# Performance work log

Measured on AMD Instinct MI355X. Metric: run time of the kernel, lower is better.

The kernel has to match this reference:

```python
import jax, jax.numpy as jnp
import numpy as np

B, C, N, H = 4, 512, 16384, 8
D = C // H
EPS = 1e-6

def setup_inputs() -> dict:
    key = jax.random.key(0)
    k1, k2, k3 = jax.random.split(key, 3)
    # xavier_normal std for Linear(C, out): sqrt(2/(fan_in+fan_out))
    std_qkv = (2.0 / (C + 3 * C)) ** 0.5
    std_proj = (2.0 / (C + C)) ** 0.5
    return {
        "x": jax.random.normal(k1, (B, C, N), dtype=jnp.float32),
        "W_qkv": jax.random.normal(k2, (C, 3 * C), dtype=jnp.float32) * std_qkv,
        "b_qkv": jnp.zeros((3 * C,), dtype=jnp.float32),
        "W_proj": jax.random.normal(k3, (C, C), dtype=jnp.float32) * std_proj,
        "b_proj": jnp.zeros((C,), dtype=jnp.float32),
    }

def _phi(x):
    return jax.nn.elu(x) + 1.0

def reference(x, W_qkv, b_qkv, W_proj, b_proj):
    # x: [B, C, N] -> [B, N, C]
    xt = jnp.swapaxes(x, 1, 2)
    qkv = xt @ W_qkv + b_qkv                      # [B, N, 3C]
    q, k, v = jnp.split(qkv, 3, axis=-1)
    # [B, N, C] -> [B, H, N, D]
    def heads(t):
        return jnp.swapaxes(t.reshape(B, N, H, D), 1, 2)
    q, k, v = heads(q), heads(k), heads(v)
    q_phi = _phi(q)                               # [B, H, N, D]
    k_phi = _phi(k)
    S = jnp.einsum('bhnd,bhne->bhde', k_phi, v)   # [B, H, D, D] KV state
    k_sum = k_phi.sum(axis=-2)                    # [B, H, D]
    num = jnp.einsum('bhnd,bhde->bhne', q_phi, S) # [B, H, N, D]
    den = jnp.einsum('bhnd,bhd->bhn', q_phi, k_sum)[..., None] + EPS
    out = num / den                               # [B, H, N, D]
    out = jnp.swapaxes(out, 1, 2).reshape(B, N, C)
    out = out @ W_proj + b_proj                   # [B, N, C]
    return jnp.swapaxes(out, 1, 2)                # [B, C, N]
```

## Files before the change

kernel.cpp:

```cpp
#include <hip/hip_runtime.h>
#include <cmath>

#define B_  4
#define C_  512
#define N_  16384
#define H_  8
#define D_  64
#define C3_ 1536
#define EPS 1e-6f

#define PADA 72
#define PADT 136
#define PADO 132

typedef __attribute__((ext_vector_type(8))) short bf16x8;
typedef __attribute__((ext_vector_type(4))) float f32x4;

typedef const void __attribute__((address_space(1)))* gas_t;
typedef void __attribute__((address_space(3)))* las_t;

__device__ __forceinline__ void gld16(const void* g, void* l) {
    __builtin_amdgcn_global_load_lds((gas_t)(unsigned long long)g,
                                     (las_t)(unsigned)(unsigned long long)l,
                                     16, 0, 0);
}

__device__ __forceinline__ ushort f2bf(float f) {
    union { float f; unsigned u; } c{f};
    unsigned r = (c.u + 0x7FFF + ((c.u >> 16) & 1)) >> 16;
    return (ushort)r;
}
__device__ __forceinline__ float bf2f(ushort b) {
    union { unsigned u; float f; } c{(unsigned)b << 16};
    return c.f;
}
__device__ __forceinline__ float phi_f(float x) { return x > 0.f ? x + 1.f : __expf(x); }

__global__ __launch_bounds__(256) void k_transpose(
        const float* __restrict__ src, ushort* __restrict__ dst,
        int R, int Cc, long sStride, long dStride) {
    __shared__ ushort T[64][72];
    const long sb = (long)blockIdx.z * sStride;
    const long db = (long)blockIdx.z * dStride;
    const int c0 = blockIdx.x * 64, r0 = blockIdx.y * 64;
    const int t = threadIdx.x;
    const int ct = t & 15, rt = t >> 4;
    float4 v[4];
    #pragma unroll
    for (int k = 0; k < 4; ++k)
        v[k] = *(const float4*)(src + sb + (long)(r0 + rt * 4 + k) * Cc + c0 + ct * 4);
    #pragma unroll
    for (int j = 0; j < 4; ++j) {
        ushort pk[4];
        #pragma unroll
        for (int k = 0; k < 4; ++k) pk[k] = f2bf(((const float*)&v[k])[j]);
        *(uint2*)&T[ct * 4 + j][rt * 4] = *(uint2*)pk;
    }
    __syncthreads();
    const int c = t >> 2, rq = (t & 3) * 16;
    ushort* d = dst + db + (long)(c0 + c) * R + r0 + rq;
    *(int4*)(d)     = *(const int4*)&T[c][rq];
    *(int4*)(d + 8) = *(const int4*)&T[c][rq + 8];
}

__global__ __launch_bounds__(256) void k_kv_s(
        const ushort* __restrict__ xt, const ushort* __restrict__ Wqt,
        const float* __restrict__ bqkv, float* __restrict__ S_g,
        float* __restrict__ ksum_g) {
    const int s = blockIdx.x, h = blockIdx.y, b = blockIdx.z;
    const int tid = threadIdx.x;
    const int w = tid >> 6, ln = tid & 63, lr = ln & 15, lq = ln >> 4;
    const int bh = b * H_ + h;
    const int lrow = ln >> 3;
    const int csw  = (ln & 7) ^ lrow;
    const int sw   = lr & 7;

    __shared__ __align__(16) char smem[34816];
    ushort* AxL = (ushort*)smem;
    ushort* BwL = (ushort*)(smem + 16384);
    ushort (*kvT)[PADT] = (ushort(*)[PADT])smem;
    __shared__ float biasL[128];

    if (tid < 128) {
        int col = tid < 64 ? (512 + h * 64 + tid) : (1024 + h * 64 + (tid - 64));
        biasL[tid] = bqkv[col];
    }

    int gA[4], gB[4];
    #pragma unroll
    for (int i = 0; i < 4; ++i) {
        const int row = (w * 4 + i) * 8 + lrow;
        gA[i] = row * C_ + csw * 8;
        const int wr = row < 64 ? (512 + h * 64 + row) : (1024 + h * 64 + (row - 64));
        gB[i] = wr * C_ + csw * 8;
    }
    const long xb = (long)b * N_ * C_;

    const f32x4 FZ = {0.f, 0.f, 0.f, 0.f};
    f32x4 Sacc[4] = {FZ, FZ, FZ, FZ};
    f32x4 Kacc = FZ;
    bf16x8 ONES;
    #pragma unroll
    for (int i = 0; i < 8; ++i) ONES[i] = (short)0x3F80;

    for (int it = 0; it < 4; ++it) {
        const ushort* xa = xt + xb + (long)((s * 4 + it) * 128) * C_;
        f32x4 acc[2][8];
        #pragma unroll
        for (int mi = 0; mi < 2; mi++)
            #pragma unroll
            for (int ji = 0; ji < 8; ji++) acc[mi][ji] = FZ;

        for (int kc = 0; kc < 8; ++kc) {
            const int c0 = kc * 64;
            __syncthreads();
            #pragma unroll
            for (int i = 0; i < 4; ++i) {
                const int ch = w * 4 + i;
                gld16(xa + gA[i] + c0, AxL + ch * 512);
                gld16(Wqt + gB[i] + c0, BwL + ch * 512);
            }
            __syncthreads();
            #pragma unroll
            for (int ks = 0; ks < 2; ++ks) {
                const int cof = ((ks * 4 + lq) ^ sw) * 8;
                bf16x8 a[2], bb[8];
                #pragma unroll
                for (int mi = 0; mi < 2; mi++)
                    a[mi] = *(const bf16x8*)&AxL[(w * 32 + mi * 16 + lr) * 64 + cof];
                #pragma unroll
                for (int ji = 0; ji < 8; ji++)
                    bb[ji] = *(const bf16x8*)&BwL[(ji * 16 + lr) * 64 + cof];
                #pragma unroll
                for (int mi = 0; mi < 2; mi++)
                    #pragma unroll
                    for (int ji = 0; ji < 8; ji++)
                        acc[mi][ji] = __builtin_amdgcn_mfma_f32_16x16x32_bf16(
                            a[mi], bb[ji], acc[mi][ji], 0, 0, 0);
            }
        }
        __syncthreads();
        #pragma unroll
        for (int mi = 0; mi < 2; mi++) {
            int nl = w * 32 + mi * 16 + lq * 4;
            #pragma unroll
            for (int ji = 0; ji < 8; ji++) {
                int j = ji * 16 + lr;
                float bs = biasL[j];
                ushort pk[4];
                #pragma unroll
                for (int r = 0; r < 4; r++) {
                    float vv = acc[mi][ji][r] + bs;
                    if (j < 64) vv = phi_f(vv);
                    pk[r] = f2bf(vv);
                }
                *(uint2*)&kvT[j][nl] = *(uint2*)pk;
            }
        }
        __syncthreads();
        #pragma unroll
        for (int ks = 0; ks < 4; ++ks) {
            bf16x8 af = *(const bf16x8*)&kvT[w * 16 + lr][ks * 32 + lq * 8];
            #pragma unroll
            for (int e = 0; e < 4; e++) {
                bf16x8 bv = *(const bf16x8*)&kvT[64 + e * 16 + lr][ks * 32 + lq * 8];
                Sacc[e] = __builtin_amdgcn_mfma_f32_16x16x32_bf16(af, bv, Sacc[e], 0, 0, 0);
            }
            Kacc = __builtin_amdgcn_mfma_f32_16x16x32_bf16(af, ONES, Kacc, 0, 0, 0);
        }
    }
    #pragma unroll
    for (int e = 0; e < 4; e++)
        #pragma unroll
        for (int r = 0; r < 4; r++)
            atomicAdd(&S_g[((long)bh * 64 + w * 16 + lq * 4 + r) * 64 + e * 16 + lr],
                      Sacc[e][r]);
    if (lr == 0) {
        #pragma unroll
        for (int r = 0; r < 4; r++)
            atomicAdd(&ksum_g[bh * 64 + w * 16 + lq * 4 + r], Kacc[r]);
    }
}

__global__ void k_sfin(const float* __restrict__ S_g, const float* __restrict__ ksum_g,
                       ushort* __restrict__ SbT) {
    int bh = blockIdx.x, t = threadIdx.x;
    for (int i = t; i < 5120; i += 256) {
        int e = i >> 6, d = i & 63;
        float v = (e < 64) ? S_g[(long)bh * 4096 + d * 64 + e]
                           : (e == 64 ? ksum_g[bh * 64 + d] : 0.f);
        ushort hi = f2bf(v);
        ushort lo = f2bf(v - bf2f(hi));
        SbT[(long)bh * 10240 + i] = hi;
        SbT[(long)bh * 10240 + 5120 + i] = lo;
    }
}

__global__ __launch_bounds__(256) void k_q_attn(
        const ushort* __restrict__ xt, const ushort* __restrict__ Wqt,
        const float* __restrict__ bqkv, const ushort* __restrict__ SbT,
        ushort* __restrict__ attn) {
    const int nt = blockIdx.x, h = blockIdx.y, b = blockIdx.z;
    const int n0 = nt * 128;
    const int tid = threadIdx.x;
    const int w = tid >> 6, ln = tid & 63, lr = ln & 15, lq = ln >> 4;
    const int bh = b * H_ + h;
    const int lrow = ln >> 3, csw = (ln & 7) ^ lrow, sw = lr & 7;

    __shared__ __align__(16) ushort AxL[128 * 64];
    __shared__ __align__(16) ushort BqL[64 * 64];
    __shared__ __align__(16) ushort Sb[160][PADA];
    __shared__ float denL[128];

    #pragma unroll
    for (int p = 0; p < 5; ++p) {
        int r = p * 32 + (tid >> 3);
        *(int4*)&Sb[r][(tid & 7) * 8] =
            *(const int4*)(SbT + (long)bh * 10240 + r * 64 + (tid & 7) * 8);
    }

    int gA[4], gB[2];
    #pragma unroll
    for (int i = 0; i < 4; ++i) {
        const int row = (w * 4 + i) * 8 + lrow;
        gA[i] = (b * N_ + n0 + row) * C_ + csw * 8;
    }
    #pragma unroll
    for (int i = 0; i < 2; ++i) {
        const int j = (w * 2 + i) * 8 + lrow;
        gB[i] = (h * 64 + j) * C_ + csw * 8;
    }

    const f32x4 FZ = {0.f, 0.f, 0.f, 0.f};
    f32x4 accq[2][4];
    #pragma unroll
    for (int mi = 0; mi < 2; mi++)
        #pragma unroll
        for (int ji = 0; ji < 4; ji++) accq[mi][ji] = FZ;

    for (int kc = 0; kc < 8; ++kc) {
        const int c0 = kc * 64;
        __syncthreads();
        #pragma unroll
        for (int i = 0; i < 4; ++i)
            gld16(xt + gA[i] + c0, AxL + (w * 4 + i) * 512);
        #pragma unroll
        for (int i = 0; i < 2; ++i)
            gld16(Wqt + gB[i] + c0, BqL + (w * 2 + i) * 512);
        __syncthreads();
        #pragma unroll
        for (int ks = 0; ks < 2; ++ks) {
            const int cof = ((ks * 4 + lq) ^ sw) * 8;
            bf16x8 a[2], bb[4];
            #pragma unroll
            for (int mi = 0; mi < 2; mi++)
                a[mi] = *(const bf16x8*)&AxL[(w * 32 + mi * 16 + lr) * 64 + cof];
            #pragma unroll
            for (int ji = 0; ji < 4; ji++)
                bb[ji] = *(const bf16x8*)&BqL[(ji * 16 + lr) * 64 + cof];
            #pragma unroll
            for (int mi = 0; mi < 2; mi++)
                #pragma unroll
                for (int ji = 0; ji < 4; ji++)
                    accq[mi][ji] = __builtin_amdgcn_mfma_f32_16x16x32_bf16(
                        a[mi], bb[ji], accq[mi][ji], 0, 0, 0);
        }
    }
    __syncthreads();
    #pragma unroll
    for (int mi = 0; mi < 2; mi++) {
        int nl = w * 32 + mi * 16 + lq * 4;
        #pragma unroll
        for (int ji = 0; ji < 4; ji++) {
            int d = ji * 16 + lr;
            float bs = bqkv[h * 64 + d];
            #pragma unroll
            for (int r = 0; r < 4; r++) {
                int row = nl + r;
                AxL[row * 64 + ((((d >> 3) ^ (row & 7)) << 3) | (d & 7))] =
                    f2bf(phi_f(accq[mi][ji][r] + bs));
            }
        }
    }
    __syncthreads();
    f32x4 accn[2][5];
    #pragma unroll
    for (int mi = 0; mi < 2; mi++)
        #pragma unroll
        for (int ei = 0; ei < 5; ei++) accn[mi][ei] = FZ;
    #pragma unroll
    for (int ks = 0; ks < 2; ++ks) {
        const int cof = ((ks * 4 + lq) ^ sw) * 8;
        bf16x8 a[2];
        #pragma unroll
        for (int mi = 0; mi < 2; mi++)
            a[mi] = *(const bf16x8*)&AxL[(w * 32 + mi * 16 + lr) * 64 + cof];
        #pragma unroll
        for (int ei = 0; ei < 5; ei++) {
            bf16x8 bhi = *(const bf16x8*)&Sb[ei * 16 + lr][ks * 32 + lq * 8];
            bf16x8 blo = *(const bf16x8*)&Sb[80 + ei * 16 + lr][ks * 32 + lq * 8];
            #pragma unroll
            for (int mi = 0; mi < 2; mi++) {
                accn[mi][ei] = __builtin_amdgcn_mfma_f32_16x16x32_bf16(
                    a[mi], bhi, accn[mi][ei], 0, 0, 0);
                accn[mi][ei] = __builtin_amdgcn_mfma_f32_16x16x32_bf16(
                    a[mi], blo, accn[mi][ei], 0, 0, 0);
            }
        }
    }
    if (lr == 0) {
        #pragma unroll
        for (int mi = 0; mi < 2; mi++)
            #pragma unroll
            for (int r = 0; r < 4; r++)
                denL[w * 32 + mi * 16 + lq * 4 + r] = accn[mi][4][r] + EPS;
    }
    __syncthreads();
    #pragma unroll
    for (int mi = 0; mi < 2; mi++) {
        int nl = w * 32 + mi * 16 + lq * 4;
        #pragma unroll
        for (int ji = 0; ji < 4; ji++) {
            int e = ji * 16 + lr;
            #pragma unroll
            for (int r = 0; r < 4; r++) {
                int row = nl + r;
                AxL[row * 64 + ((((e >> 3) ^ (row & 7)) << 3) | (e & 7))] =
                    f2bf(accn[mi][ji][r] / denL[row]);
            }
        }
    }
    __syncthreads();
    {
        int row = tid >> 1, co = (tid & 1) * 32;
        int4* dp = (int4*)(attn + ((long)(b * N_ + n0 + row)) * C_ + h * 64 + co);
        #pragma unroll
        for (int k = 0; k < 4; ++k)
            dp[k] = *(const int4*)&AxL[row * 64 + ((((co >> 3) + k) ^ (row & 7)) << 3)];
    }
}

__global__ __launch_bounds__(256) void k_proj(
        const ushort* __restrict__ attn, const ushort* __restrict__ Wpt,
        const float* __restrict__ bproj, float* __restrict__ out) {
    const int nt = blockIdx.x, jt = blockIdx.y;
    const int tid = threadIdx.x;
    const int w = tid >> 6, ln = tid & 63, lr = ln & 15, lq = ln >> 4;
    const int b = nt >> 7;
    const int nloc = (nt & 127) * 128;
    const int lrow = ln >> 3, csw = (ln & 7) ^ lrow, sw = lr & 7;

    __shared__ __align__(16) char smem[36864];
    ushort* AaL = (ushort*)smem;
    ushort* BwL = (ushort*)(smem + 16384);
    float (*outT)[PADO] = (float(*)[PADO])smem;

    int gA[4], gB[4];
    #pragma unroll
    for (int i = 0; i < 4; ++i) {
        const int row = (w * 4 + i) * 8 + lrow;
        gA[i] = (nt * 128 + row) * C_ + csw * 8;
        gB[i] = (jt * 128 + row) * C_ + csw * 8;
    }

    const f32x4 FZ = {0.f, 0.f, 0.f, 0.f};
    f32x4 acc[2][8];
    #pragma unroll
    for (int mi = 0; mi < 2; mi++)
        #pragma unroll
        for (int ji = 0; ji < 8; ji++) acc[mi][ji] = FZ;

    for (int kc = 0; kc < 8; ++kc) {
        const int c0 = kc * 64;
        __syncthreads();
        #pragma unroll
        for (int i = 0; i < 4; ++i) {
            const int ch = w * 4 + i;
            gld16(attn + gA[i] + c0, AaL + ch * 512);
            gld16(Wpt + gB[i] + c0, BwL + ch * 512);
        }
        __syncthreads();
        #pragma unroll
        for (int ks = 0; ks < 2; ++ks) {
            const int cof = ((ks * 4 + lq) ^ sw) * 8;
            bf16x8 a[2], bb[8];
            #pragma unroll
            for (int mi = 0; mi < 2; mi++)
                a[mi] = *(const bf16x8*)&AaL[(w * 32 + mi * 16 + lr) * 64 + cof];
            #pragma unroll
            for (int ji = 0; ji < 8; ji++)
                bb[ji] = *(const bf16x8*)&BwL[(ji * 16 + lr) * 64 + cof];
            #pragma unroll
            for (int mi = 0; mi < 2; mi++)
                #pragma unroll
                for (int ji = 0; ji < 8; ji++)
                    acc[mi][ji] = __builtin_amdgcn_mfma_f32_16x16x32_bf16(
                        a[mi], bb[ji], acc[mi][ji], 0, 0, 0);
        }
    }
    #pragma unroll
    for (int half = 0; half < 2; ++half) {
        __syncthreads();
        #pragma unroll
        for (int mi = 0; mi < 2; mi++) {
            int nl = w * 32 + mi * 16 + lq * 4;
            #pragma unroll
            for (int ji = 0; ji < 4; ji++) {
                int cl = ji * 16 + lr;
                float bs = bproj[jt * 128 + half * 64 + cl];
                f32x4 v = acc[mi][half * 4 + ji];
                #pragma unroll
                for (int r = 0; r < 4; r++) v[r] += bs;
                *(f32x4*)&outT[cl][nl] = v;
            }
        }
        __syncthreads();
        {
            int cl = tid >> 2, ch = (tid & 3) * 32;
            const float* sp = &outT[cl][ch];
            float* dp = out + ((long)(b * C_ + jt * 128 + half * 64 + cl)) * N_ + nloc + ch;
            #pragma unroll
            for (int k = 0; k < 8; ++k)
                ((float4*)dp)[k] = ((const float4*)sp)[k];
        }
    }
}

__global__ __launch_bounds__(256) void kernelA_fb(
        const float* __restrict__ x, const float* __restrict__ Wqkv,
        const float* __restrict__ bqkv, float* __restrict__ S_g,
        float* __restrict__ ksum_g) {
    const int h = blockIdx.x;
    const int s = blockIdx.y;
    const int b = blockIdx.z;
    const int tid = threadIdx.x;
    const int tn = tid & 15;
    const int tj = tid >> 4;
    const int td = tid & 15;
    const int te = tid >> 4;

    __shared__ float As[16][64];
    __shared__ float Bs[16][128];
    __shared__ float kphi_s[64][64];
    __shared__ float v_s[64][64];

    float acc2[4][4];
    #pragma unroll
    for (int i = 0; i < 4; i++)
        #pragma unroll
        for (int j = 0; j < 4; j++) acc2[i][j] = 0.f;
    float ksum_r = 0.f;

    float bias_j[8];
    #pragma unroll
    for (int jj = 0; jj < 8; jj++) {
        int j = tj * 8 + jj;
        int col = (j < 64) ? (512 + h * 64 + j) : (1024 + h * 64 + (j - 64));
        bias_j[jj] = bqkv[col];
    }

    for (int it = 0; it < 8; ++it) {
        const int n0 = (s * 8 + it) * 64;
        float acc[4][8];
        #pragma unroll
        for (int i = 0; i < 4; i++)
            #pragma unroll
            for (int jj = 0; jj < 8; jj++) acc[i][jj] = 0.f;

        for (int kc = 0; kc < 32; ++kc) {
            const int c0 = kc * 16;
            __syncthreads();
            {
                int r = tid >> 4, n4 = (tid & 15) * 4;
                const float* src = x + ((size_t)b * C_ + (c0 + r)) * (size_t)N_ + n0 + n4;
                *(float4*)&As[r][n4] = *(const float4*)src;
            }
            #pragma unroll
            for (int part = 0; part < 2; ++part) {
                int idx = tid + part * 256;
                int r = idx >> 5;
                int j4 = (idx & 31) * 4;
                int col = (j4 < 64) ? (512 + h * 64 + j4) : (1024 + h * 64 + (j4 - 64));
                const float* src = Wqkv + (size_t)(c0 + r) * C3_ + col;
                *(float4*)&Bs[r][j4] = *(const float4*)src;
            }
            __syncthreads();
            #pragma unroll
            for (int k = 0; k < 16; ++k) {
                float a[4], bb[8];
                *(float4*)a      = *(const float4*)&As[k][tn * 4];
                *(float4*)&bb[0] = *(const float4*)&Bs[k][tj * 8];
                *(float4*)&bb[4] = *(const float4*)&Bs[k][tj * 8 + 4];
                #pragma unroll
                for (int i = 0; i < 4; i++)
                    #pragma unroll
                    for (int jj = 0; jj < 8; jj++)
                        acc[i][jj] = fmaf(a[i], bb[jj], acc[i][jj]);
            }
        }
        __syncthreads();
        if (tj < 8) {
            #pragma unroll
            for (int i = 0; i < 4; i++) {
                int n = tn * 4 + i;
                float tmp[8];
                #pragma unroll
                for (int jj = 0; jj < 8; jj++) tmp[jj] = phi_f(acc[i][jj] + bias_j[jj]);
                *(float4*)&kphi_s[n][tj * 8]     = *(float4*)&tmp[0];
                *(float4*)&kphi_s[n][tj * 8 + 4] = *(float4*)&tmp[4];
            }
        } else {
            #pragma unroll
            for (int i = 0; i < 4; i++) {
                int n = tn * 4 + i;
                float tmp[8];
                #pragma unroll
                for (int jj = 0; jj < 8; jj++) tmp[jj] = acc[i][jj] + bias_j[jj];
                *(float4*)&v_s[n][(tj - 8) * 8]     = *(float4*)&tmp[0];
                *(float4*)&v_s[n][(tj - 8) * 8 + 4] = *(float4*)&tmp[4];
            }
        }
        __syncthreads();
        #pragma unroll 4
        for (int n = 0; n < 64; ++n) {
            float a[4], bb[4];
            *(float4*)a  = *(const float4*)&kphi_s[n][td * 4];
            *(float4*)bb = *(const float4*)&v_s[n][te * 4];
            #pragma unroll
            for (int dd = 0; dd < 4; dd++)
                #pragma unroll
                for (int ee = 0; ee < 4; ee++)
                    acc2[dd][ee] = fmaf(a[dd], bb[ee], acc2[dd][ee]);
        }
        if (tid < 64) {
            float sum = 0.f;
            #pragma unroll 8
            for (int n = 0; n < 64; ++n) sum += kphi_s[n][tid];
            ksum_r += sum;
        }
    }

    const int bh = b * H_ + h;
    #pragma unroll
    for (int dd = 0; dd < 4; dd++)
        #pragma unroll
        for (int ee = 0; ee < 4; ee++)
            atomicAdd(&S_g[((size_t)bh * 64 + td * 4 + dd) * 64 + te * 4 + ee], acc2[dd][ee]);
    if (tid < 64) atomicAdd(&ksum_g[bh * 64 + tid], ksum_r);
}

__global__ __launch_bounds__(256) void kernelB_fb(
        const float* __restrict__ x, const float* __restrict__ Wqkv,
        const float* __restrict__ bqkv, const float* __restrict__ Wproj,
        const float* __restrict__ bproj, const float* __restrict__ S_g,
        const float* __restrict__ ksum_g, float* __restrict__ out) {
    const int nt = blockIdx.x;
    const int b  = blockIdx.y;
    const int n0 = nt * 16;
    const int tid = threadIdx.x;
    const int tn = tid & 3;
    const int tj = tid >> 2;

    __shared__ float QA[512][16];
    __shared__ float As[16][16];
    __shared__ float Bs2[16][256];
    __shared__ float SB[16][64];
    __shared__ float ksumL[512];
    __shared__ float denL[16];

    ksumL[tid]       = ksum_g[(size_t)b * 512 + tid];
    ksumL[tid + 256] = ksum_g[(size_t)b * 512 + tid + 256];

    for (int half = 0; half < 2; ++half) {
        float acc[4][4];
        #pragma unroll
        for (int i = 0; i < 4; i++)
            #pragma unroll
            for (int j = 0; j < 4; j++) acc[i][j] = 0.f;

        for (int kc = 0; kc < 32; ++kc) {
            const int c0 = kc * 16;
            __syncthreads();
            {
                int r = tid >> 4, n = tid & 15;
                As[r][n] = x[((size_t)b * C_ + c0 + r) * (size_t)N_ + n0 + n];
            }
            {
                int r = tid >> 4;
                int j0 = (tid & 15) * 16;
                const float* src = Wqkv + (size_t)(c0 + r) * C3_ + half * 256 + j0;
                float4* dst = (float4*)&Bs2[r][j0];
                #pragma unroll
                for (int q4 = 0; q4 < 4; q4++) dst[q4] = ((const float4*)src)[q4];
            }
            __syncthreads();
            #pragma unroll
            for (int k = 0; k < 16; ++k) {
                float a[4], bb[4];
                *(float4*)a  = *(const float4*)&As[k][tn * 4];
                *(float4*)bb = *(const float4*)&Bs2[k][tj * 4];
                #pragma unroll
                for (int i = 0; i < 4; i++)
                    #pragma unroll
                    for (int jj = 0; jj < 4; jj++)
                        acc[i][jj] = fmaf(a[i], bb[jj], acc[i][jj]);
            }
        }
        #pragma unroll
        for (int jj = 0; jj < 4; jj++) {
            int c = half * 256 + tj * 4 + jj;
            float bq = bqkv[c];
            float tmp[4];
            #pragma unroll
            for (int i = 0; i < 4; i++) tmp[i] = phi_f(acc[i][jj] + bq);
            *(float4*)&QA[c][tn * 4] = *(float4*)tmp;
        }
    }
    __syncthreads();

    for (int h = 0; h < H_; ++h) {
        if (tid < 16) {
            float d = 0.f;
            #pragma unroll 8
            for (int dd = 0; dd < 64; ++dd)
                d = fmaf(QA[h * 64 + dd][tid], ksumL[h * 64 + dd], d);
            denL[tid] = d + EPS;
        }
        float acc4[4] = {0.f, 0.f, 0.f, 0.f};
        for (int dc = 0; dc < 4; ++dc) {
            __syncthreads();
            {
                int r = tid >> 4, e4 = (tid & 15) * 4;
                *(float4*)&SB[r][e4] =
                    *(const float4*)&S_g[(((size_t)(b * H_ + h)) * 64 + dc * 16 + r) * 64 + e4];
            }
            __syncthreads();
            #pragma unroll
            for (int k = 0; k < 16; ++k) {
                float a[4];
                *(float4*)a = *(const float4*)&QA[h * 64 + dc * 16 + k][tn * 4];
                float bb = SB[k][tj];
                #pragma unroll
                for (int i = 0; i < 4; i++) acc4[i] = fmaf(a[i], bb, acc4[i]);
            }
        }
        __syncthreads();
        {
            float tmp[4];
            #pragma unroll
            for (int i = 0; i < 4; i++) tmp[i] = acc4[i] / denL[tn * 4 + i];
            *(float4*)&QA[h * 64 + tj][tn * 4] = *(float4*)tmp;
        }
        __syncthreads();
    }

    for (int half = 0; half < 2; ++half) {
        float acc[4][4];
        #pragma unroll
        for (int i = 0; i < 4; i++)
            #pragma unroll
            for (int j = 0; j < 4; j++) acc[i][j] = 0.f;

        for (int kc = 0; kc < 32; ++kc) {
            __syncthreads();
            {
                int r = tid >> 4;
                int j0 = (tid & 15) * 16;
                const float* src = Wproj + (size_t)(kc * 16 + r) * C_ + half * 256 + j0;
                float4* dst = (float4*)&Bs2[r][j0];
                #pragma unroll
                for (int q4 = 0; q4 < 4; q4++) dst[q4] = ((const float4*)src)[q4];
            }
            __syncthreads();
            #pragma unroll
            for (int k = 0; k < 16; ++k) {
                float a[4], bb[4];
                *(float4*)a  = *(const float4*)&QA[kc * 16 + k][tn * 4];
                *(float4*)bb = *(const float4*)&Bs2[k][tj * 4];
                #pragma unroll
                for (int i = 0; i < 4; i++)
                    #pragma unroll
                    for (int jj = 0; jj < 4; jj++)
                        acc[i][jj] = fmaf(a[i], bb[jj], acc[i][jj]);
            }
        }
        #pragma unroll
        for (int jj = 0; jj < 4; jj++) {
            int c = half * 256 + tj * 4 + jj;
            float bp = bproj[c];
            float tmp[4];
            #pragma unroll
            for (int i = 0; i < 4; i++) tmp[i] = acc[i][jj] + bp;
            *(float4*)&out[((size_t)b * C_ + c) * (size_t)N_ + n0 + tn * 4] = *(float4*)tmp;
        }
    }
}

extern "C" void kernel_launch(void* const* d_in, const int* in_sizes, int n_in,
                              void* d_out, int out_size, void* d_ws, size_t ws_size,
                              hipStream_t stream) {
    const float* x     = (const float*)d_in[0];
    const float* Wqkv  = (const float*)d_in[1];
    const float* bqkv  = (const float*)d_in[2];
    const float* Wproj = (const float*)d_in[3];
    const float* bproj = (const float*)d_in[4];
    float* out = (float*)d_out;

    const size_t oS    = 0;
    const size_t oK    = oS + 524288;
    const size_t oXT   = oK + 8192;
    const size_t oWq   = oXT + 67108864;
    const size_t oWp   = oWq + 1572864;
    const size_t oSbT  = oWp + 524288;
    const size_t oAttn = oSbT + 655360;
    const size_t need  = oAttn + 67108864;

    float* S_g    = (float*)((char*)d_ws + oS);
    float* ksum_g = (float*)((char*)d_ws + oK);

    if (ws_size < need) {
        hipMemsetAsync(d_ws, 0, 532480, stream);
        kernelA_fb<<<dim3(H_, 32, B_), 256, 0, stream>>>(x, Wqkv, bqkv, S_g, ksum_g);
        kernelB_fb<<<dim3(N_ / 16, B_), 256, 0, stream>>>(x, Wqkv, bqkv, Wproj, bproj,
                                                          S_g, ksum_g, out);
        return;
    }

    ushort* xt   = (ushort*)((char*)d_ws + oXT);
    ushort* Wqt  = (ushort*)((char*)d_ws + oWq);
    ushort* Wpt  = (ushort*)((char*)d_ws + oWp);
    ushort* SbT  = (ushort*)((char*)d_ws + oSbT);
    ushort* attn = (ushort*)((char*)d_ws + oAttn);

    hipMemsetAsync(d_ws, 0, 532480, stream);
    k_transpose<<<dim3(N_ / 64, C_ / 64, B_), 256, 0, stream>>>(
        x, xt, C_, N_, (long)C_ * N_, (long)N_ * C_);
    k_transpose<<<dim3(C3_ / 64, C_ / 64, 1), 256, 0, stream>>>(
        Wqkv, Wqt, C_, C3_, 0, 0);
    k_transpose<<<dim3(C_ / 64, C_ / 64, 1), 256, 0, stream>>>(
        Wproj, Wpt, C_, C_, 0, 0);
    k_kv_s<<<dim3(32, H_, B_), 256, 0, stream>>>(xt, Wqt, bqkv, S_g, ksum_g);
    k_sfin<<<dim3(B_ * H_), 256, 0, stream>>>(S_g, ksum_g, SbT);
    k_q_attn<<<dim3(N_ / 128, H_, B_), 256, 0, stream>>>(xt, Wqt, bqkv, SbT, attn);
    k_proj<<<dim3((B_ * N_) / 128, 4), 256, 0, stream>>>(attn, Wpt, bproj, out);
}
```

Measured before the change: 576.5 us.

## Double-buffer LDS tiles in the three GEMM kernels and halve kv grid

Converts the K-loop of k_kv_s, k_q_attn and k_proj to a ping-pong LDS scheme, so the global_load_lds of the next 64-wide chunk is issued while MFMAs run on the current chunk. This removes one barrier per chunk and overlaps memory latency with compute. k_kv_s also processes 8 row tiles per block instead of 4 with half the grid, which halves the atomic traffic into S. The cost is larger LDS (64KB per block for kv and proj), which lowers occupancy, and fewer blocks for the kv stage.

```diff
diff --git a/kernel.cpp b/kernel.cpp
--- a/kernel.cpp
+++ b/kernel.cpp
@@ -75,9 +75,11 @@
     const int csw  = (ln & 7) ^ lrow;
     const int sw   = lr & 7;
 
-    __shared__ __align__(16) char smem[34816];
-    ushort* AxL = (ushort*)smem;
-    ushort* BwL = (ushort*)(smem + 16384);
+    __shared__ __align__(16) char smem[65536];
+    ushort* A0 = (ushort*)smem;
+    ushort* B0 = (ushort*)(smem + 16384);
+    ushort* A1 = (ushort*)(smem + 32768);
+    ushort* B1 = (ushort*)(smem + 49152);
     ushort (*kvT)[PADT] = (ushort(*)[PADT])smem;
     __shared__ float biasL[128];
 
@@ -103,34 +105,33 @@
     #pragma unroll
     for (int i = 0; i < 8; ++i) ONES[i] = (short)0x3F80;
 
-    for (int it = 0; it < 4; ++it) {
-        const ushort* xa = xt + xb + (long)((s * 4 + it) * 128) * C_;
+    for (int it = 0; it < 8; ++it) {
+        const ushort* xa = xt + xb + (long)((s * 8 + it) * 128) * C_;
         f32x4 acc[2][8];
         #pragma unroll
         for (int mi = 0; mi < 2; mi++)
             #pragma unroll
             for (int ji = 0; ji < 8; ji++) acc[mi][ji] = FZ;
 
-        for (int kc = 0; kc < 8; ++kc) {
-            const int c0 = kc * 64;
-            __syncthreads();
+        auto stage = [&](ushort* Ab, ushort* Bb, int c0) {
             #pragma unroll
             for (int i = 0; i < 4; ++i) {
                 const int ch = w * 4 + i;
-                gld16(xa + gA[i] + c0, AxL + ch * 512);
-                gld16(Wqt + gB[i] + c0, BwL + ch * 512);
-            }
-            __syncthreads();
+                gld16(xa + gA[i] + c0, Ab + ch * 512);
+                gld16(Wqt + gB[i] + c0, Bb + ch * 512);
+            }
+        };
+        auto compute = [&](const ushort* Ab, const ushort* Bb) {
             #pragma unroll
             for (int ks = 0; ks < 2; ++ks) {
                 const int cof = ((ks * 4 + lq) ^ sw) * 8;
                 bf16x8 a[2], bb[8];
                 #pragma unroll
                 for (int mi = 0; mi < 2; mi++)
-                    a[mi] = *(const bf16x8*)&AxL[(w * 32 + mi * 16 + lr) * 64 + cof];
+                    a[mi] = *(const bf16x8*)&Ab[(w * 32 + mi * 16 + lr) * 64 + cof];
                 #pragma unroll
                 for (int ji = 0; ji < 8; ji++)
-                    bb[ji] = *(const bf16x8*)&BwL[(ji * 16 + lr) * 64 + cof];
+                    bb[ji] = *(const bf16x8*)&Bb[(ji * 16 + lr) * 64 + cof];
                 #pragma unroll
                 for (int mi = 0; mi < 2; mi++)
                     #pragma unroll
@@ -138,8 +139,19 @@
                         acc[mi][ji] = __builtin_amdgcn_mfma_f32_16x16x32_bf16(
                             a[mi], bb[ji], acc[mi][ji], 0, 0, 0);
             }
-        }
-        __syncthreads();
+        };
+
+        stage(A0, B0, 0);
+        __syncthreads();
+        #pragma unroll
+        for (int kc = 0; kc < 8; kc += 2) {
+            stage(A1, B1, (kc + 1) * 64);
+            compute(A0, B0);
+            __syncthreads();
+            if (kc + 2 < 8) stage(A0, B0, (kc + 2) * 64);
+            compute(A1, B1);
+            __syncthreads();
+        }
         #pragma unroll
         for (int mi = 0; mi < 2; mi++) {
             int nl = w * 32 + mi * 16 + lq * 4;
@@ -168,6 +180,7 @@
             }
             Kacc = __builtin_amdgcn_mfma_f32_16x16x32_bf16(af, ONES, Kacc, 0, 0, 0);
         }
+        __syncthreads();
     }
     #pragma unroll
     for (int e = 0; e < 4; e++)
@@ -207,8 +220,11 @@
     const int bh = b * H_ + h;
     const int lrow = ln >> 3, csw = (ln & 7) ^ lrow, sw = lr & 7;
 
-    __shared__ __align__(16) ushort AxL[128 * 64];
-    __shared__ __align__(16) ushort BqL[64 * 64];
+    __shared__ __align__(16) char smem[49152];
+    ushort* A0 = (ushort*)smem;
+    ushort* A1 = (ushort*)(smem + 16384);
+    ushort* Q0 = (ushort*)(smem + 32768);
+    ushort* Q1 = (ushort*)(smem + 40960);
     __shared__ __align__(16) ushort Sb[160][PADA];
     __shared__ float denL[128];
 
@@ -238,26 +254,25 @@
         #pragma unroll
         for (int ji = 0; ji < 4; ji++) accq[mi][ji] = FZ;
 
-    for (int kc = 0; kc < 8; ++kc) {
-        const int c0 = kc * 64;
-        __syncthreads();
+    auto stage = [&](ushort* Ab, ushort* Bb, int c0) {
         #pragma unroll
         for (int i = 0; i < 4; ++i)
-            gld16(xt + gA[i] + c0, AxL + (w * 4 + i) * 512);
+            gld16(xt + gA[i] + c0, Ab + (w * 4 + i) * 512);
         #pragma unroll
         for (int i = 0; i < 2; ++i)
-            gld16(Wqt + gB[i] + c0, BqL + (w * 2 + i) * 512);
-        __syncthreads();
+            gld16(Wqt + gB[i] + c0, Bb + (w * 2 + i) * 512);
+    };
+    auto compute = [&](const ushort* Ab, const ushort* Bb) {
         #pragma unroll
         for (int ks = 0; ks < 2; ++ks) {
             const int cof = ((ks * 4 + lq) ^ sw) * 8;
             bf16x8 a[2], bb[4];
             #pragma unroll
             for (int mi = 0; mi < 2; mi++)
-                a[mi] = *(const bf16x8*)&AxL[(w * 32 + mi * 16 + lr) * 64 + cof];
+                a[mi] = *(const bf16x8*)&Ab[(w * 32 + mi * 16 + lr) * 64 + cof];
             #pragma unroll
             for (int ji = 0; ji < 4; ji++)
-                bb[ji] = *(const bf16x8*)&BqL[(ji * 16 + lr) * 64 + cof];
+                bb[ji] = *(const bf16x8*)&Bb[(ji * 16 + lr) * 64 + cof];
             #pragma unroll
             for (int mi = 0; mi < 2; mi++)
                 #pragma unroll
@@ -265,8 +280,19 @@
                     accq[mi][ji] = __builtin_amdgcn_mfma_f32_16x16x32_bf16(
                         a[mi], bb[ji], accq[mi][ji], 0, 0, 0);
         }
-    }
+    };
+
+    stage(A0, Q0, 0);
     __syncthreads();
+    #pragma unroll
+    for (int kc = 0; kc < 8; kc += 2) {
+        stage(A1, Q1, (kc + 1) * 64);
+        compute(A0, Q0);
+        __syncthreads();
+        if (kc + 2 < 8) stage(A0, Q0, (kc + 2) * 64);
+        compute(A1, Q1);
+        __syncthreads();
+    }
     #pragma unroll
     for (int mi = 0; mi < 2; mi++) {
         int nl = w * 32 + mi * 16 + lq * 4;
@@ -277,7 +303,7 @@
             #pragma unroll
             for (int r = 0; r < 4; r++) {
                 int row = nl + r;
-                AxL[row * 64 + ((((d >> 3) ^ (row & 7)) << 3) | (d & 7))] =
+                A0[row * 64 + ((((d >> 3) ^ (row & 7)) << 3) | (d & 7))] =
                     f2bf(phi_f(accq[mi][ji][r] + bs));
             }
         }
@@ -294,7 +320,7 @@
         bf16x8 a[2];
         #pragma unroll
         for (int mi = 0; mi < 2; mi++)
-            a[mi] = *(const bf16x8*)&AxL[(w * 32 + mi * 16 + lr) * 64 + cof];
+            a[mi] = *(const bf16x8*)&A0[(w * 32 + mi * 16 + lr) * 64 + cof];
         #pragma unroll
         for (int ei = 0; ei < 5; ei++) {
             bf16x8 bhi = *(const bf16x8*)&Sb[ei * 16 + lr][ks * 32 + lq * 8];
@@ -325,7 +351,7 @@
             #pragma unroll
             for (int r = 0; r < 4; r++) {
                 int row = nl + r;
-                AxL[row * 64 + ((((e >> 3) ^ (row & 7)) << 3) | (e & 7))] =
+                A0[row * 64 + ((((e >> 3) ^ (row & 7)) << 3) | (e & 7))] =
                     f2bf(accn[mi][ji][r] / denL[row]);
             }
         }
@@ -336,7 +362,7 @@
         int4* dp = (int4*)(attn + ((long)(b * N_ + n0 + row)) * C_ + h * 64 + co);
         #pragma unroll
         for (int k = 0; k < 4; ++k)
-            dp[k] = *(const int4*)&AxL[row * 64 + ((((co >> 3) + k) ^ (row & 7)) << 3)];
+            dp[k] = *(const int4*)&A0[row * 64 + ((((co >> 3) + k) ^ (row & 7)) << 3)];
     }
 }
 
@@ -350,9 +376,11 @@
     const int nloc = (nt & 127) * 128;
     const int lrow = ln >> 3, csw = (ln & 7) ^ lrow, sw = lr & 7;
 
-    __shared__ __align__(16) char smem[36864];
-    ushort* AaL = (ushort*)smem;
-    ushort* BwL = (ushort*)(smem + 16384);
+    __shared__ __align__(16) char smem[65536];
+    ushort* A0 = (ushort*)smem;
+    ushort* B0 = (ushort*)(smem + 16384);
+    ushort* A1 = (ushort*)(smem + 32768);
+    ushort* B1 = (ushort*)(smem + 49152);
     float (*outT)[PADO] = (float(*)[PADO])smem;
 
     int gA[4], gB[4];
@@ -370,26 +398,25 @@
         #pragma unroll
         for (int ji = 0; ji < 8; ji++) acc[mi][ji] = FZ;
 
-    for (int kc = 0; kc < 8; ++kc) {
-        const int c0 = kc * 64;
-        __syncthreads();
+    auto stage = [&](ushort* Ab, ushort* Bb, int c0) {
         #pragma unroll
         for (int i = 0; i < 4; ++i) {
             const int ch = w * 4 + i;
-            gld16(attn + gA[i] + c0, AaL + ch * 512);
-            gld16(Wpt + gB[i] + c0, BwL + ch * 512);
-        }
-        __syncthreads();
+            gld16(attn + gA[i] + c0, Ab + ch * 512);
+            gld16(Wpt + gB[i] + c0, Bb + ch * 512);
+        }
+    };
+    auto compute = [&](const ushort* Ab, const ushort* Bb) {
         #pragma unroll
         for (int ks = 0; ks < 2; ++ks) {
             const int cof = ((ks * 4 + lq) ^ sw) * 8;
             bf16x8 a[2], bb[8];
             #pragma unroll
             for (int mi = 0; mi < 2; mi++)
-                a[mi] = *(const bf16x8*)&AaL[(w * 32 + mi * 16 + lr) * 64 + cof];
+                a[mi] = *(const bf16x8*)&Ab[(w * 32 + mi * 16 + lr) * 64 + cof];
             #pragma unroll
             for (int ji = 0; ji < 8; ji++)
-                bb[ji] = *(const bf16x8*)&BwL[(ji * 16 + lr) * 64 + cof];
+                bb[ji] = *(const bf16x8*)&Bb[(ji * 16 + lr) * 64 + cof];
             #pragma unroll
             for (int mi = 0; mi < 2; mi++)
                 #pragma unroll
@@ -397,10 +424,22 @@
                     acc[mi][ji] = __builtin_amdgcn_mfma_f32_16x16x32_bf16(
                         a[mi], bb[ji], acc[mi][ji], 0, 0, 0);
         }
+    };
+
+    stage(A0, B0, 0);
+    __syncthreads();
+    #pragma unroll
+    for (int kc = 0; kc < 8; kc += 2) {
+        stage(A1, B1, (kc + 1) * 64);
+        compute(A0, B0);
+        __syncthreads();
+        if (kc + 2 < 8) stage(A0, B0, (kc + 2) * 64);
+        compute(A1, B1);
+        __syncthreads();
     }
     #pragma unroll
     for (int half = 0; half < 2; ++half) {
-        __syncthreads();
+        if (half) __syncthreads();
         #pragma unroll
         for (int mi = 0; mi < 2; mi++) {
             int nl = w * 32 + mi * 16 + lq * 4;
@@ -739,7 +778,7 @@
         Wqkv, Wqt, C_, C3_, 0, 0);
     k_transpose<<<dim3(C_ / 64, C_ / 64, 1), 256, 0, stream>>>(
         Wproj, Wpt, C_, C_, 0, 0);
-    k_kv_s<<<dim3(32, H_, B_), 256, 0, stream>>>(xt, Wqt, bqkv, S_g, ksum_g);
+    k_kv_s<<<dim3(16, H_, B_), 256, 0, stream>>>(xt, Wqt, bqkv, S_g, ksum_g);
     k_sfin<<<dim3(B_ * H_), 256, 0, stream>>>(S_g, ksum_g, SbT);
     k_q_attn<<<dim3(N_ / 128, H_, B_), 256, 0, stream>>>(xt, Wqt, bqkv, SbT, attn);
     k_proj<<<dim3((B_ * N_) / 128, 4), 256, 0, stream>>>(attn, Wpt, bproj, out);
```

Measured after the change: 522.0 us. -9.5%, faster.
